# Kernel tuning notes

Measured on AMD Instinct MI355X. Metric: run time of the kernel, lower is better.

Reference implementation:

```python
import jax, jax.numpy as jnp
import numpy as np

N, D = 8192, 128

def _rbf_kernel(x, y):
    # InfoVAE-style kernel: exp(-mean((x_i - y_j)^2) / dim) = exp(-sqdist / dim^2)
    dim = x.shape[1]
    x2 = jnp.sum(x * x, axis=1)              # [n]
    y2 = jnp.sum(y * y, axis=1)              # [m]
    sqdist = x2[:, None] + y2[None, :] - 2.0 * (x @ y.T)  # [n, m]
    return jnp.exp(-sqdist / (dim * dim))


def setup_inputs() -> dict:
    key = jax.random.key(0)
    k1, k2 = jax.random.split(key)
    inputs = jax.random.normal(k1, (N, D), dtype=jnp.float32)
    true_samples = jax.random.normal(k2, (N, D), dtype=jnp.float32)
    return {"inputs": inputs, "true_samples": true_samples}


def reference(inputs, true_samples):
    x = true_samples  # samples from standard normal prior
    y = inputs
    k_xx = _rbf_kernel(x, x)
    k_yy = _rbf_kernel(y, y)
    k_xy = _rbf_kernel(x, y)
    mmd = jnp.mean(k_xx) + jnp.mean(k_yy) - 2.0 * jnp.mean(k_xy)
    return mmd
```

## Files before the change

### kernel.cpp

```cpp
#include <hip/hip_runtime.h>
#include <hip/hip_bf16.h>
#include <math.h>


#define NN 8192
#define DD 128
#define TZ 16384
#define SPLIT 16
#define NBLK (64 * SPLIT)

typedef __attribute__((ext_vector_type(8))) short bf16x8;
typedef __attribute__((ext_vector_type(4))) float f32x4;
typedef __attribute__((ext_vector_type(2))) float f32x2;

#if __has_builtin(__builtin_amdgcn_exp2f)
#define EXP2F __builtin_amdgcn_exp2f
#else
#define EXP2F exp2f
#endif

constexpr float LOG2E = 0x1.715476p+0f;
constexpr float S2 = LOG2E / 8192.0f;

constexpr size_t PLANE = 1048576;

#define LDS_RED 32768

constexpr size_t WS_CTR  = 2048;
constexpr size_t WS_NORM = 2560;
constexpr size_t WS_Z    = WS_NORM + (size_t)TZ * sizeof(float);

__device__ __forceinline__ void gload_lds16(const void* g, void* l) {
  __builtin_amdgcn_global_load_lds(
      (const __attribute__((address_space(1))) void*)g,
      (__attribute__((address_space(3))) void*)l, 16, 0, 0);
}

__global__ __launch_bounds__(256) void prep(
    const float* __restrict__ X, const float* __restrict__ Y,
    char* __restrict__ Zs, float* __restrict__ normZ,
    double* __restrict__ sums, unsigned* __restrict__ ctr) {
  if (blockIdx.x == 0) {
    sums[threadIdx.x] = 0.0;
    if (threadIdx.x == 0) *ctr = 0u;
  }

  const int row = blockIdx.x * 4 + (threadIdx.x >> 6);
  const int lane = threadIdx.x & 63;
  const float* __restrict__ src =
      (row < NN) ? (X + (size_t)row * DD) : (Y + (size_t)(row - NN) * DD);
  const float2 v = *reinterpret_cast<const float2*>(src + 2 * lane);

  float n = v.x * v.x + v.y * v.y;

  const int ks = lane >> 4;
  const int quadc = (lane >> 2) & 3;
  const int inner = (lane & 3) * 4;
  char* dst = Zs + (size_t)ks * PLANE + (size_t)row * 64 +
              ((quadc ^ ((row >> 1) & 3)) << 4) + inner;
  *reinterpret_cast<__hip_bfloat162*>(dst) =
      __hip_bfloat162{__float2bfloat16(v.x), __float2bfloat16(v.y)};

#pragma unroll
  for (int o = 32; o > 0; o >>= 1) n += __shfl_down(n, o);
  if (lane == 0) normZ[row] = n * (-LOG2E / 16384.0f);
}

__global__ __launch_bounds__(256, 4) void mmd_mfma(
    const char* __restrict__ Zs, const float* __restrict__ normZ,
    double* __restrict__ sums, unsigned* __restrict__ ctr,
    float* __restrict__ out) {
  __shared__ alignas(16) char lds[LDS_RED + 64];

  const int bid = blockIdx.x;
  const int p = bid / SPLIT, s = bid % SPLIT;
  const int q = 127 - p;
  const int n1 = (127 - p - s) / SPLIT + 1;
  const int u0 = s + SPLIT * n1 - (128 - p);
  const int n2 = (u0 <= p) ? (p - u0) / SPLIT + 1 : 0;

  const int segI[2]  = {p, q};
  const int segJ0[2] = {p + s, q + u0};
  const int segN[2]  = {n1, n2};

  const int tid = threadIdx.x;
  const int lane = tid & 63, wave = tid >> 6;
  const int wr = wave >> 1, wc = wave & 1;
  const int lr = lane & 15, quad = lane >> 4;

  const int csw = (quad ^ ((lr >> 1) & 3)) << 4;
  const char* aRd = lds + (wr * 64 + lr) * 64 + csw;
  const size_t bOff = (size_t)(wc * 64 + lr) * 64 + csw;

  bf16x8 a[4], b[4];

#define LOADA(ks) do {                                                      \
    _Pragma("unroll")                                                       \
    for (int i = 0; i < 4; ++i)                                             \
      a[i] = *reinterpret_cast<const bf16x8*>(aRd + (ks) * 8192 + i * 1024);\
  } while (0)

#define LOADB(base, pl) do {                                                \
    _Pragma("unroll")                                                       \
    for (int j = 0; j < 4; ++j)                                             \
      b[j] = *reinterpret_cast<const bf16x8*>(                              \
          (base) + (size_t)(pl) * PLANE + j * 1024);                        \
  } while (0)

#define MFMAS() do {                                                        \
    _Pragma("unroll")                                                       \
    for (int i = 0; i < 4; ++i)                                             \
      _Pragma("unroll")                                                     \
      for (int j = 0; j < 4; ++j)                                           \
        acc[i][j] = __builtin_amdgcn_mfma_f32_16x16x32_bf16(                \
            a[i], b[j], acc[i][j], 0, 0, 0);                                \
  } while (0)

  const f32x2 s2v = {S2, S2};
  double blockAcc = 0.0;

  for (int seg = 0; seg < 2; ++seg) {
    const int I = segI[seg];
    const int nIter = segN[seg];
    if (nIter == 0) continue;
    int J = segJ0[seg];

    const char* srcA0 = Zs + (size_t)(I * 128 + wave * 32) * 64 + lane * 16;
    char* ldwA = lds + wave * 2048;
#pragma unroll
    for (int ks = 0; ks < 4; ++ks) {
      gload_lds16(srcA0 + (size_t)ks * PLANE,        ldwA + ks * 8192);
      gload_lds16(srcA0 + (size_t)ks * PLANE + 1024, ldwA + ks * 8192 + 1024);
    }

    const char* bbase = Zs + (size_t)J * 8192 + bOff;
    LOADB(bbase, 0);
    asm volatile("s_waitcnt vmcnt(0)\n\ts_barrier" ::: "memory");

    const float* nzA = normZ + I * 128 + wr * 64;

    for (int it = 0; it < nIter; ++it) {
      const char* bnext = (it + 1 < nIter) ? bbase + SPLIT * 8192 : bbase;
      f32x4 acc[4][4] = {};

      LOADA(0);
      __builtin_amdgcn_sched_barrier(0);
      MFMAS();
      __builtin_amdgcn_sched_barrier(0);
      LOADB(bbase, 1);

      LOADA(1);
      __builtin_amdgcn_sched_barrier(0);
      MFMAS();
      __builtin_amdgcn_sched_barrier(0);
      LOADB(bbase, 2);

      LOADA(2);
      __builtin_amdgcn_sched_barrier(0);
      MFMAS();
      __builtin_amdgcn_sched_barrier(0);
      LOADB(bbase, 3);

      LOADA(3);
      __builtin_amdgcn_sched_barrier(0);
      MFMAS();
      __builtin_amdgcn_sched_barrier(0);
      LOADB(bnext, 0);

      f32x4 ar[4];
#pragma unroll
      for (int i = 0; i < 4; ++i)
        ar[i] = *reinterpret_cast<const f32x4*>(nzA + i * 16 + quad * 4);
      const float* nzB = normZ + J * 128 + wc * 64;
      float cb[4];
#pragma unroll
      for (int j = 0; j < 4; ++j) cb[j] = nzB[j * 16 + lr];

      f32x2 part01 = {0.f, 0.f}, part23 = {0.f, 0.f};
#pragma unroll
      for (int i = 0; i < 4; ++i) {
        const f32x2 ar01 = {ar[i].x, ar[i].y};
        const f32x2 ar23 = {ar[i].z, ar[i].w};
#pragma unroll
        for (int j = 0; j < 4; ++j) {
          const f32x2 rb2 = {cb[j], cb[j]};
          const f32x2 base01 = ar01 + rb2;
          const f32x2 base23 = ar23 + rb2;
          const f32x2 acc01 = {acc[i][j][0], acc[i][j][1]};
          const f32x2 acc23 = {acc[i][j][2], acc[i][j][3]};
          const f32x2 arg01 = __builtin_elementwise_fma(acc01, s2v, base01);
          const f32x2 arg23 = __builtin_elementwise_fma(acc23, s2v, base23);
          part01 += (f32x2){EXP2F(arg01.x), EXP2F(arg01.y)};
          part23 += (f32x2){EXP2F(arg23.x), EXP2F(arg23.y)};
        }
      }
      const f32x2 ps = part01 + part23;
      double w = ((I < 64) == (J < 64)) ? 1.0 : -1.0;
      if (I != J) w += w;
      blockAcc += (double)(ps.x + ps.y) * w;

      J += SPLIT;
      bbase = bnext;
    }

    __syncthreads();
  }

#undef LOADA
#undef LOADB
#undef MFMAS

  __shared__ double red[4];
  __shared__ int lastFlag;
#pragma unroll
  for (int o = 32; o > 0; o >>= 1) blockAcc += __shfl_down(blockAcc, o);
  if (lane == 0) red[wave] = blockAcc;
  __syncthreads();
  if (tid == 0) {
    atomicAdd(&sums[bid & 255], red[0] + red[1] + red[2] + red[3]);
    __threadfence();
    lastFlag = (atomicAdd(ctr, 1u) == NBLK - 1);
  }
  __syncthreads();
  if (wave == 0 && lastFlag) {
    double v = 0.0;
#pragma unroll
    for (int k = 0; k < 4; ++k)
      v += atomicAdd(&sums[lane * 4 + k], 0.0);
#pragma unroll
    for (int o = 32; o > 0; o >>= 1) v += __shfl_down(v, o);
    if (lane == 0)
      out[0] = (float)(v * (1.0 / ((double)NN * (double)NN)));
  }
}

extern "C" void kernel_launch(void* const* d_in, const int* in_sizes, int n_in,
                              void* d_out, int out_size, void* d_ws, size_t ws_size,
                              hipStream_t stream) {
  const float* y_inputs = (const float*)d_in[0];
  const float* x_true   = (const float*)d_in[1];
  float* out = (float*)d_out;

  char* ws = (char*)d_ws;
  double* sums = (double*)ws;
  unsigned* ctr = (unsigned*)(ws + WS_CTR);
  float* normZ = (float*)(ws + WS_NORM);
  char* Zs = ws + WS_Z;

  prep<<<TZ / 4, 256, 0, stream>>>(x_true, y_inputs, Zs, normZ, sums, ctr);
  mmd_mfma<<<NBLK, 256, 0, stream>>>(Zs, normZ, sums, ctr, out);
}
```

Before: 121.4 us.

## Double-buffer B fragments, hoist row norms, raise MFMA priority, retune split

B operand registers are now double-buffered, so each global load of a B plane is issued two MFMA stages before it is consumed instead of one, giving more latency hiding. The per-row norm loads are moved out of the inner loop to once per segment, and MFMA blocks are wrapped in s_setprio to favour matrix issue. SPLIT drops from 16 to 12, which reduces the block count and gives each block more tiles, and launch bounds drop to 3 blocks per CU to make room for the extra registers. The trade is lower occupancy and fewer blocks, which may hurt load balance or latency hiding across waves.

```diff
diff --git a/kernel.cpp b/kernel.cpp
--- a/kernel.cpp
+++ b/kernel.cpp
@@ -6,7 +6,7 @@
 #define NN 8192
 #define DD 128
 #define TZ 16384
-#define SPLIT 16
+#define SPLIT 12
 #define NBLK (64 * SPLIT)
 
 typedef __attribute__((ext_vector_type(8))) short bf16x8;
@@ -66,7 +66,7 @@
   if (lane == 0) normZ[row] = n * (-LOG2E / 16384.0f);
 }
 
-__global__ __launch_bounds__(256, 4) void mmd_mfma(
+__global__ __launch_bounds__(256, 3) void mmd_mfma(
     const char* __restrict__ Zs, const float* __restrict__ normZ,
     double* __restrict__ sums, unsigned* __restrict__ ctr,
     float* __restrict__ out) {
@@ -92,7 +92,8 @@
   const char* aRd = lds + (wr * 64 + lr) * 64 + csw;
   const size_t bOff = (size_t)(wc * 64 + lr) * 64 + csw;
 
-  bf16x8 a[4], b[4];
+  bf16x8 a[4], b0[4], b1[4];
+  f32x4 ar[4];
 
 #define LOADA(ks) do {                                                      \
     _Pragma("unroll")                                                       \
@@ -100,20 +101,22 @@
       a[i] = *reinterpret_cast<const bf16x8*>(aRd + (ks) * 8192 + i * 1024);\
   } while (0)
 
-#define LOADB(base, pl) do {                                                \
+#define LOADB(dst, base, pl) do {                                           \
     _Pragma("unroll")                                                       \
     for (int j = 0; j < 4; ++j)                                             \
-      b[j] = *reinterpret_cast<const bf16x8*>(                              \
+      dst[j] = *reinterpret_cast<const bf16x8*>(                            \
           (base) + (size_t)(pl) * PLANE + j * 1024);                        \
   } while (0)
 
-#define MFMAS() do {                                                        \
+#define MFMAS(bb) do {                                                      \
+    __builtin_amdgcn_s_setprio(1);                                          \
     _Pragma("unroll")                                                       \
     for (int i = 0; i < 4; ++i)                                             \
       _Pragma("unroll")                                                     \
       for (int j = 0; j < 4; ++j)                                           \
         acc[i][j] = __builtin_amdgcn_mfma_f32_16x16x32_bf16(                \
-            a[i], b[j], acc[i][j], 0, 0, 0);                                \
+            a[i], bb[j], acc[i][j], 0, 0, 0);                               \
+    __builtin_amdgcn_s_setprio(0);                                          \
   } while (0)
 
   const f32x2 s2v = {S2, S2};
@@ -125,6 +128,11 @@
     if (nIter == 0) continue;
     int J = segJ0[seg];
 
+    const float* nzA = normZ + I * 128 + wr * 64;
+#pragma unroll
+    for (int i = 0; i < 4; ++i)
+      ar[i] = *reinterpret_cast<const f32x4*>(nzA + i * 16 + quad * 4);
+
     const char* srcA0 = Zs + (size_t)(I * 128 + wave * 32) * 64 + lane * 16;
     char* ldwA = lds + wave * 2048;
 #pragma unroll
@@ -134,10 +142,9 @@
     }
 
     const char* bbase = Zs + (size_t)J * 8192 + bOff;
-    LOADB(bbase, 0);
+    LOADB(b0, bbase, 0);
+    LOADB(b1, bbase, 1);
     asm volatile("s_waitcnt vmcnt(0)\n\ts_barrier" ::: "memory");
-
-    const float* nzA = normZ + I * 128 + wr * 64;
 
     for (int it = 0; it < nIter; ++it) {
       const char* bnext = (it + 1 < nIter) ? bbase + SPLIT * 8192 : bbase;
@@ -145,32 +152,28 @@
 
       LOADA(0);
       __builtin_amdgcn_sched_barrier(0);
-      MFMAS();
-      __builtin_amdgcn_sched_barrier(0);
-      LOADB(bbase, 1);
+      MFMAS(b0);
+      __builtin_amdgcn_sched_barrier(0);
+      LOADB(b0, bbase, 2);
 
       LOADA(1);
       __builtin_amdgcn_sched_barrier(0);
-      MFMAS();
-      __builtin_amdgcn_sched_barrier(0);
-      LOADB(bbase, 2);
+      MFMAS(b1);
+      __builtin_amdgcn_sched_barrier(0);
+      LOADB(b1, bbase, 3);
 
       LOADA(2);
       __builtin_amdgcn_sched_barrier(0);
-      MFMAS();
-      __builtin_amdgcn_sched_barrier(0);
-      LOADB(bbase, 3);
+      MFMAS(b0);
+      __builtin_amdgcn_sched_barrier(0);
+      LOADB(b0, bnext, 0);
 
       LOADA(3);
       __builtin_amdgcn_sched_barrier(0);
-      MFMAS();
-      __builtin_amdgcn_sched_barrier(0);
-      LOADB(bnext, 0);
-
-      f32x4 ar[4];
-#pragma unroll
-      for (int i = 0; i < 4; ++i)
-        ar[i] = *reinterpret_cast<const f32x4*>(nzA + i * 16 + quad * 4);
+      MFMAS(b1);
+      __builtin_amdgcn_sched_barrier(0);
+      LOADB(b1, bnext, 1);
+
       const float* nzB = normZ + J * 128 + wc * 64;
       float cb[4];
 #pragma unroll
```

Measured after the change: 110.4 us. -9.1%, faster.
